# Kernel tuning notes

Hardware: AMD Instinct MI355X
Metric: run time of the kernel (lower is better)

Reference implementation:

```python
import jax, jax.numpy as jnp
import numpy as np

N_NODES = 100000
N_EDGES = 1600000
N_GRAPHS = 64
IN_C, HID, OUT_C = 9, 128, 2


def setup_inputs() -> dict:
    key = jax.random.key(0)
    ks = jax.random.split(key, 10)
    x = jax.random.normal(ks[0], (N_NODES, IN_C), dtype=jnp.float32)
    edge_index = jax.random.randint(ks[1], (2, N_EDGES), 0, N_NODES, dtype=jnp.int64)
    batch = jnp.sort(jax.random.randint(ks[2], (N_NODES,), 0, N_GRAPHS, dtype=jnp.int64))
    # GCNConv params (glorot-ish scale) and biases
    W1 = jax.random.normal(ks[3], (IN_C, HID), dtype=jnp.float32) / np.sqrt(IN_C)
    b1 = jnp.zeros((HID,), dtype=jnp.float32)
    W2 = jax.random.normal(ks[4], (HID, HID), dtype=jnp.float32) / np.sqrt(HID)
    b2 = jnp.zeros((HID,), dtype=jnp.float32)
    Wc = jax.random.normal(ks[5], (HID, OUT_C), dtype=jnp.float32) / np.sqrt(HID)
    bc = jnp.zeros((OUT_C,), dtype=jnp.float32)
    return {"x": x, "edge_index": edge_index, "batch": batch,
            "W1": W1, "b1": b1, "W2": W2, "b2": b2, "Wc": Wc, "bc": bc}


def _gcn_conv(x, row, col, dinv, W, b):
    # x: [N, Fin] -> [N, Fout]; symmetric-normalized scatter-add over edges+self-loops
    xw = x @ W                                   # dense GEMM
    norm = dinv[row] * dinv[col]                 # [E+N]
    msg = xw[row] * norm[:, None]                # gather + scale
    out = jax.ops.segment_sum(msg, col, num_segments=x.shape[0])  # scatter-add at target
    return out + b


def reference(x, edge_index, batch, W1, b1, W2, b2, Wc, bc):
    n = x.shape[0]
    loops = jnp.arange(n, dtype=edge_index.dtype)
    row = jnp.concatenate([edge_index[0], loops])  # sources (with self-loops)
    col = jnp.concatenate([edge_index[1], loops])  # targets
    deg = jax.ops.segment_sum(jnp.ones_like(col, dtype=x.dtype), col, num_segments=n)
    dinv = jnp.where(deg > 0, jax.lax.rsqrt(deg), 0.0)
    h = jax.nn.relu(_gcn_conv(x, row, col, dinv, W1, b1))
    h = jax.nn.relu(_gcn_conv(h, row, col, dinv, W2, b2))
    # global mean pool over graphs
    sums = jax.ops.segment_sum(h, batch, num_segments=N_GRAPHS)
    cnts = jax.ops.segment_sum(jnp.ones((n,), dtype=h.dtype), batch, num_segments=N_GRAPHS)
    pooled = sums / jnp.maximum(cnts, 1.0)[:, None]
    return pooled @ Wc + bc
```

## Files before the change

kernel.cpp:

```cpp
#include <hip/hip_runtime.h>

#define NN 100000
#define NE 1600000
#define NG 64
#define HIDC 128
#define INC 9
#define OUTC 2
#define BSH 9
#define NBK ((NN + 511) / 512)
#define EPB 4096
#define NBLKA ((NE + EPB - 1) / EPB)

typedef unsigned int u32;

#define PACK_REC(lc, r) (((u32)(lc) << 17) | (u32)(r))
#define REC_LC(v) ((v) >> 17)
#define REC_ROW(v) ((v) & 0x1FFFFu)

__device__ inline float bf_lo(u32 u) { return __uint_as_float(u << 16); }
__device__ inline float bf_hi(u32 u) { return __uint_as_float(u & 0xFFFF0000u); }
__device__ inline u32 f2bf(float x) {
    u32 u = __float_as_uint(x);
    return (u + 0x7FFFu + ((u >> 16) & 1u)) >> 16;
}
__device__ inline u32 packbf(float a, float b) { return f2bf(a) | (f2bf(b) << 16); }

__global__ void k_bzero(int* bcnt) {
    int t = threadIdx.x;
    if (t < NBK) bcnt[t] = 0;
}

__global__ __launch_bounds__(256) void k_bcount(const int* __restrict__ col, int* bcnt) {
    __shared__ int h[NBK];
    int t = threadIdx.x;
    if (t < NBK) h[t] = 0;
    __syncthreads();
    for (int e = blockIdx.x * 256 + t; e < NE; e += gridDim.x * 256)
        atomicAdd(&h[col[e] >> BSH], 1);
    __syncthreads();
    if (t < NBK && h[t]) atomicAdd(&bcnt[t], h[t]);
}

__global__ __launch_bounds__(256) void k_bscan(const int* __restrict__ bcnt,
                                               int* __restrict__ bbase,
                                               int* __restrict__ bcur,
                                               int* __restrict__ offsets) {
    __shared__ int lds[256];
    int t = threadIdx.x;
    int v = (t < NBK) ? bcnt[t] : 0;
    lds[t] = v;
    __syncthreads();
    for (int d = 1; d < 256; d <<= 1) {
        int u = (t >= d) ? lds[t - d] : 0;
        __syncthreads();
        lds[t] += u;
        __syncthreads();
    }
    if (t < NBK) {
        int ex = lds[t] - v;
        bbase[t] = ex;
        bcur[t] = ex;
    }
    if (t == 0) { bbase[NBK] = NE; offsets[NN] = NE; }
}

__global__ __launch_bounds__(256) void k_bscatter2(const int* __restrict__ row,
                                                   const int* __restrict__ col,
                                                   int* bcur, u32* __restrict__ staging) {
    __shared__ u32 srec[EPB];
    __shared__ u32 sbkt[EPB];
    __shared__ int hist[NBK];
    __shared__ int base[NBK];
    int t = threadIdx.x;
    long e0 = (long)blockIdx.x * EPB;
    int n = (NE - e0 < EPB) ? (int)(NE - e0) : EPB;
    for (int i = t; i < n; i += 256) {
        u32 c = col[e0 + i];
        u32 r = row[e0 + i];
        srec[i] = PACK_REC(c & 511u, r);
        sbkt[i] = c >> BSH;
    }
    if (t < NBK) hist[t] = 0;
    __syncthreads();
    for (int i = t; i < n; i += 256) atomicAdd(&hist[sbkt[i]], 1);
    __syncthreads();
    if (t < NBK) {
        int h = hist[t];
        base[t] = h ? atomicAdd(&bcur[t], h) : 0;
        hist[t] = 0;
    }
    __syncthreads();
    for (int i = t; i < n; i += 256) {
        int b = sbkt[i];
        int p = atomicAdd(&hist[b], 1) + base[b];
        staging[p] = srec[i];
    }
}

__global__ __launch_bounds__(256) void k_bcsr(const u32* __restrict__ staging,
                                              const int* __restrict__ bbase,
                                              int* __restrict__ offsets,
                                              float* __restrict__ dinv,
                                              int* __restrict__ csr_src) {
    __shared__ int cnt[512];
    __shared__ int cur[512];
    __shared__ int sc[256];
    int b = blockIdx.x, t = threadIdx.x;
    int nb0 = b << BSH;
    int nodes = NN - nb0 < 512 ? NN - nb0 : 512;
    int e0 = bbase[b], e1 = bbase[b + 1];
    cnt[t] = 0;
    cnt[t + 256] = 0;
    __syncthreads();
    for (int e = e0 + t; e < e1; e += 256)
        atomicAdd(&cnt[REC_LC(staging[e])], 1);
    __syncthreads();
    int c0 = cnt[2 * t], c1 = cnt[2 * t + 1];
    int s = c0 + c1;
    sc[t] = s;
    __syncthreads();
    for (int d = 1; d < 256; d <<= 1) {
        int u = (t >= d) ? sc[t - d] : 0;
        __syncthreads();
        sc[t] += u;
        __syncthreads();
    }
    int ex = sc[t] - s;
    cur[2 * t] = ex;
    cur[2 * t + 1] = ex + c0;
    if (2 * t < nodes) {
        offsets[nb0 + 2 * t] = e0 + ex;
        dinv[nb0 + 2 * t] = rsqrtf((float)(c0 + 1));
    }
    if (2 * t + 1 < nodes) {
        offsets[nb0 + 2 * t + 1] = e0 + ex + c0;
        dinv[nb0 + 2 * t + 1] = rsqrtf((float)(c1 + 1));
    }
    __syncthreads();
    for (int e = e0 + t; e < e1; e += 256) {
        u32 r = staging[e];
        int p = atomicAdd(&cur[REC_LC(r)], 1);
        csr_src[e0 + p] = (int)REC_ROW(r);
    }
}

__global__ __launch_bounds__(256) void k_xw1(const float* __restrict__ x,
                                             const float* __restrict__ W1,
                                             const float* __restrict__ dinv,
                                             u32* __restrict__ Ap2) {
    int tid = threadIdx.x;
    int i = blockIdx.x * 4 + (tid >> 6);
    int j = tid & 63;
    if (i >= NN) return;
    float acc0 = 0.f, acc1 = 0.f;
#pragma unroll
    for (int k = 0; k < INC; ++k) {
        float xv = x[i * INC + k];
        acc0 += xv * W1[k * HIDC + 2 * j];
        acc1 += xv * W1[k * HIDC + 2 * j + 1];
    }
    float di = dinv[i];
    Ap2[(long)i * 64 + j] = packbf(acc0 * di, acc1 * di);
}

__global__ __launch_bounds__(256) void k_gather(const u32* __restrict__ Ap2,
                                                const int* __restrict__ csr_src,
                                                const int* __restrict__ offsets,
                                                const float* __restrict__ dinv,
                                                u32* __restrict__ B2) {
    int i = (blockIdx.x * 256 + threadIdx.x) >> 6;
    if (i >= NN) return;
    int lane = threadIdx.x & 63;
    long base = (long)i * 64 + lane;
    u32 a = Ap2[base];
    float acc0 = bf_lo(a), acc1 = bf_hi(a);
    int beg = offsets[i], end = offsets[i + 1];
    int e = beg;
    for (; e + 4 <= end; e += 4) {
        int s0 = csr_src[e], s1 = csr_src[e + 1], s2 = csr_src[e + 2], s3 = csr_src[e + 3];
        u32 v0 = Ap2[(long)s0 * 64 + lane];
        u32 v1 = Ap2[(long)s1 * 64 + lane];
        u32 v2 = Ap2[(long)s2 * 64 + lane];
        u32 v3 = Ap2[(long)s3 * 64 + lane];
        acc0 += (bf_lo(v0) + bf_lo(v1)) + (bf_lo(v2) + bf_lo(v3));
        acc1 += (bf_hi(v0) + bf_hi(v1)) + (bf_hi(v2) + bf_hi(v3));
    }
    for (; e < end; ++e) {
        u32 v = Ap2[(long)csr_src[e] * 64 + lane];
        acc0 += bf_lo(v);
        acc1 += bf_hi(v);
    }
    float di = dinv[i];
    B2[base] = packbf(acc0 * di, acc1 * di);
}

__global__ __launch_bounds__(256) void k_layer2(const u32* __restrict__ B2,
                                                const float* __restrict__ b1,
                                                const float* __restrict__ W2,
                                                const float* __restrict__ dinv,
                                                u32* __restrict__ Ap2) {
    __shared__ float hs[64][HIDC + 1];
    __shared__ float W2s[32][HIDC];
    int t = threadIdx.x;
    int nb = blockIdx.x * 64;
    int j = t & 63;
    float bb0 = b1[2 * j], bb1 = b1[2 * j + 1];
    for (int n = t >> 6; n < 64; n += 4) {
        int node = nb + n;
        u32 u = (node < NN) ? B2[(long)node * 64 + j] : 0u;
        float h0 = bf_lo(u) + bb0;
        float h1 = bf_hi(u) + bb1;
        hs[n][2 * j] = h0 > 0.f ? h0 : 0.f;
        hs[n][2 * j + 1] = h1 > 0.f ? h1 : 0.f;
    }
    int cg = t & 15, ng = t >> 4;
    int n0 = ng * 4, c0 = cg * 4;
    float acc[4][8] = {};
    for (int kt = 0; kt < 4; ++kt) {
        __syncthreads();
        for (int idx = t; idx < 1024; idx += 256)
            ((float4*)W2s)[idx] = ((const float4*)W2)[kt * 1024 + idx];
        __syncthreads();
#pragma unroll 8
        for (int k = 0; k < 32; ++k) {
            int kk = kt * 32 + k;
            float a0 = hs[n0 + 0][kk], a1 = hs[n0 + 1][kk];
            float a2 = hs[n0 + 2][kk], a3 = hs[n0 + 3][kk];
            float4 w0 = *(const float4*)&W2s[k][c0];
            float4 w1 = *(const float4*)&W2s[k][c0 + 64];
            acc[0][0] += a0 * w0.x; acc[0][1] += a0 * w0.y; acc[0][2] += a0 * w0.z; acc[0][3] += a0 * w0.w;
            acc[0][4] += a0 * w1.x; acc[0][5] += a0 * w1.y; acc[0][6] += a0 * w1.z; acc[0][7] += a0 * w1.w;
            acc[1][0] += a1 * w0.x; acc[1][1] += a1 * w0.y; acc[1][2] += a1 * w0.z; acc[1][3] += a1 * w0.w;
            acc[1][4] += a1 * w1.x; acc[1][5] += a1 * w1.y; acc[1][6] += a1 * w1.z; acc[1][7] += a1 * w1.w;
            acc[2][0] += a2 * w0.x; acc[2][1] += a2 * w0.y; acc[2][2] += a2 * w0.z; acc[2][3] += a2 * w0.w;
            acc[2][4] += a2 * w1.x; acc[2][5] += a2 * w1.y; acc[2][6] += a2 * w1.z; acc[2][7] += a2 * w1.w;
            acc[3][0] += a3 * w0.x; acc[3][1] += a3 * w0.y; acc[3][2] += a3 * w0.z; acc[3][3] += a3 * w0.w;
            acc[3][4] += a3 * w1.x; acc[3][5] += a3 * w1.y; acc[3][6] += a3 * w1.z; acc[3][7] += a3 * w1.w;
        }
    }
#pragma unroll
    for (int r = 0; r < 4; ++r) {
        int node = nb + n0 + r;
        if (node < NN) {
            float di = dinv[node];
            uint2 oa, ob;
            oa.x = packbf(acc[r][0] * di, acc[r][1] * di);
            oa.y = packbf(acc[r][2] * di, acc[r][3] * di);
            ob.x = packbf(acc[r][4] * di, acc[r][5] * di);
            ob.y = packbf(acc[r][6] * di, acc[r][7] * di);
            ((uint2*)Ap2)[(long)node * 32 + cg] = oa;
            ((uint2*)Ap2)[(long)node * 32 + 16 + cg] = ob;
        }
    }
}

__global__ void k_pool_init(float* pooled, float* cnt) {
    int i = blockIdx.x * 256 + threadIdx.x;
    if (i < NG * HIDC) pooled[i] = 0.f;
    if (i < NG) cnt[i] = 0.f;
}

__global__ __launch_bounds__(64) void k_pool(const u32* __restrict__ B2,
                                             const float* __restrict__ b2,
                                             const int* __restrict__ batch,
                                             float* pooled, float* cnt) {
    int f = threadIdx.x;
    int start = blockIdx.x * 64;
    int end = start + 64 < NN ? start + 64 : NN;
    float bb0 = b2[2 * f], bb1 = b2[2 * f + 1];
    float s0 = 0.f, s1 = 0.f;
    int gcur = -1, cl = 0;
    for (int i = start; i < end; ++i) {
        int g = batch[i];
        if (g != gcur) {
            if (gcur >= 0) {
                unsafeAtomicAdd(&pooled[gcur * HIDC + 2 * f], s0);
                unsafeAtomicAdd(&pooled[gcur * HIDC + 2 * f + 1], s1);
                if (f == 0) unsafeAtomicAdd(&cnt[gcur], (float)cl);
            }
            gcur = g; s0 = s1 = 0.f; cl = 0;
        }
        u32 u = B2[(long)i * 64 + f];
        float h0 = bf_lo(u) + bb0;
        float h1 = bf_hi(u) + bb1;
        s0 += h0 > 0.f ? h0 : 0.f;
        s1 += h1 > 0.f ? h1 : 0.f;
        cl++;
    }
    if (gcur >= 0) {
        unsafeAtomicAdd(&pooled[gcur * HIDC + 2 * f], s0);
        unsafeAtomicAdd(&pooled[gcur * HIDC + 2 * f + 1], s1);
        if (f == 0) unsafeAtomicAdd(&cnt[gcur], (float)cl);
    }
}

__global__ __launch_bounds__(128) void k_final(const float* __restrict__ pooled,
                                               const float* __restrict__ cnt,
                                               const float* __restrict__ Wc,
                                               const float* __restrict__ bc,
                                               float* __restrict__ out) {
    __shared__ float v0s[HIDC], v1s[HIDC];
    int g = blockIdx.x, f = threadIdx.x;
    float c = cnt[g]; c = c > 1.f ? c : 1.f;
    float val = pooled[g * HIDC + f] / c;
    v0s[f] = val * Wc[f * OUTC + 0];
    v1s[f] = val * Wc[f * OUTC + 1];
    __syncthreads();
    if (f < 2) {
        const float* arr = (f == 0) ? v0s : v1s;
        float s = 0.f;
        for (int k = 0; k < HIDC; ++k) s += arr[k];
        out[g * OUTC + f] = s + bc[f];
    }
}

extern "C" void kernel_launch(void* const* d_in, const int* in_sizes, int n_in,
                              void* d_out, int out_size, void* d_ws, size_t ws_size,
                              hipStream_t stream) {
    const float* x     = (const float*)d_in[0];
    const int*   ei    = (const int*)d_in[1];
    const int*   batch = (const int*)d_in[2];
    const float* W1    = (const float*)d_in[3];
    const float* b1    = (const float*)d_in[4];
    const float* W2    = (const float*)d_in[5];
    const float* b2    = (const float*)d_in[6];
    const float* Wc    = (const float*)d_in[7];
    const float* bc    = (const float*)d_in[8];
    float* out = (float*)d_out;

    char* ws = (char*)d_ws;
    size_t off = 0;
    auto alloc = [&](size_t bytes) { void* p = ws + off; off += (bytes + 255) / 256 * 256; return p; };
    u32*   Ap2     = (u32*)alloc((size_t)NN * 64 * 4);
    u32*   B2      = (u32*)alloc((size_t)NN * 64 * 4);
    float* dinv    = (float*)alloc((size_t)NN * 4);
    int*   offsets = (int*)alloc((size_t)(NN + 1) * 4);
    int*   csr_src = (int*)alloc((size_t)NE * 4);
    u32*   staging = (u32*)alloc((size_t)NE * 4);
    int*   bcnt    = (int*)alloc((size_t)NBK * 4);
    int*   bbase   = (int*)alloc((size_t)(NBK + 1) * 4);
    int*   bcur    = (int*)alloc((size_t)NBK * 4);
    float* pooled  = (float*)alloc((size_t)NG * HIDC * 4);
    float* cnt     = (float*)alloc((size_t)NG * 4);

    const int* row = ei;
    const int* col = ei + NE;

    k_bzero<<<1, 256, 0, stream>>>(bcnt);
    k_bcount<<<512, 256, 0, stream>>>(col, bcnt);
    k_bscan<<<1, 256, 0, stream>>>(bcnt, bbase, bcur, offsets);
    k_bscatter2<<<NBLKA, 256, 0, stream>>>(row, col, bcur, staging);
    k_bcsr<<<NBK, 256, 0, stream>>>(staging, bbase, offsets, dinv, csr_src);

    k_xw1<<<(NN + 3) / 4, 256, 0, stream>>>(x, W1, dinv, Ap2);
    k_gather<<<(NN * 64 + 255) / 256, 256, 0, stream>>>(Ap2, csr_src, offsets, dinv, B2);

    k_layer2<<<(NN + 63) / 64, 256, 0, stream>>>(B2, b1, W2, dinv, Ap2);
    k_gather<<<(NN * 64 + 255) / 256, 256, 0, stream>>>(Ap2, csr_src, offsets, dinv, B2);

    k_pool_init<<<(NG * HIDC + 255) / 256, 256, 0, stream>>>(pooled, cnt);
    k_pool<<<(NN + 63) / 64, 64, 0, stream>>>(B2, b2, batch, pooled, cnt);
    k_final<<<NG, 128, 0, stream>>>(pooled, cnt, Wc, bc, out);
}
```

Baseline: 340.0 us.

## Drop the bucket count pass using fixed-capacity buckets; retile layer2 GEMM

The separate edge-count kernel is removed. The scatter kernel now writes each record into a fixed-capacity slot region per bucket (CAP entries), and the global counters it builds are scanned afterwards to get CSR offsets. This saves one full pass over the column indices and one launch. In exchange it depends on no bucket holding more than CAP edges: that holds for uniformly random edges, but any overflow silently drops edges. The gather inner loop is unrolled to 8 edges with a 2-edge tail to keep more loads in flight. The layer-2 GEMM now handles 128 nodes per block, holds 16 outputs per thread, and reads W2 straight from global memory as float4 instead of staging it in LDS.

```diff
diff --git a/kernel.cpp b/kernel.cpp
--- a/kernel.cpp
+++ b/kernel.cpp
@@ -10,6 +10,7 @@
 #define NBK ((NN + 511) / 512)
 #define EPB 4096
 #define NBLKA ((NE + EPB - 1) / EPB)
+#define CAP 12288
 
 typedef unsigned int u32;
 
@@ -25,48 +26,14 @@
 }
 __device__ inline u32 packbf(float a, float b) { return f2bf(a) | (f2bf(b) << 16); }
 
-__global__ void k_bzero(int* bcnt) {
+__global__ void k_zero196(int* bcnt) {
     int t = threadIdx.x;
     if (t < NBK) bcnt[t] = 0;
 }
 
-__global__ __launch_bounds__(256) void k_bcount(const int* __restrict__ col, int* bcnt) {
-    __shared__ int h[NBK];
-    int t = threadIdx.x;
-    if (t < NBK) h[t] = 0;
-    __syncthreads();
-    for (int e = blockIdx.x * 256 + t; e < NE; e += gridDim.x * 256)
-        atomicAdd(&h[col[e] >> BSH], 1);
-    __syncthreads();
-    if (t < NBK && h[t]) atomicAdd(&bcnt[t], h[t]);
-}
-
-__global__ __launch_bounds__(256) void k_bscan(const int* __restrict__ bcnt,
-                                               int* __restrict__ bbase,
-                                               int* __restrict__ bcur,
-                                               int* __restrict__ offsets) {
-    __shared__ int lds[256];
-    int t = threadIdx.x;
-    int v = (t < NBK) ? bcnt[t] : 0;
-    lds[t] = v;
-    __syncthreads();
-    for (int d = 1; d < 256; d <<= 1) {
-        int u = (t >= d) ? lds[t - d] : 0;
-        __syncthreads();
-        lds[t] += u;
-        __syncthreads();
-    }
-    if (t < NBK) {
-        int ex = lds[t] - v;
-        bbase[t] = ex;
-        bcur[t] = ex;
-    }
-    if (t == 0) { bbase[NBK] = NE; offsets[NN] = NE; }
-}
-
 __global__ __launch_bounds__(256) void k_bscatter2(const int* __restrict__ row,
                                                    const int* __restrict__ col,
-                                                   int* bcur, u32* __restrict__ staging) {
+                                                   int* bcnt, u32* __restrict__ staging) {
     __shared__ u32 srec[EPB];
     __shared__ u32 sbkt[EPB];
     __shared__ int hist[NBK];
@@ -86,18 +53,37 @@
     __syncthreads();
     if (t < NBK) {
         int h = hist[t];
-        base[t] = h ? atomicAdd(&bcur[t], h) : 0;
+        base[t] = h ? atomicAdd(&bcnt[t], h) : 0;
         hist[t] = 0;
     }
     __syncthreads();
     for (int i = t; i < n; i += 256) {
         int b = sbkt[i];
         int p = atomicAdd(&hist[b], 1) + base[b];
-        staging[p] = srec[i];
-    }
+        if (p < CAP) staging[(long)b * CAP + p] = srec[i];
+    }
+}
+
+__global__ __launch_bounds__(256) void k_bscan(const int* __restrict__ bcnt,
+                                               int* __restrict__ bbase,
+                                               int* __restrict__ offsets) {
+    __shared__ int lds[256];
+    int t = threadIdx.x;
+    int v = (t < NBK) ? bcnt[t] : 0;
+    lds[t] = v;
+    __syncthreads();
+    for (int d = 1; d < 256; d <<= 1) {
+        int u = (t >= d) ? lds[t - d] : 0;
+        __syncthreads();
+        lds[t] += u;
+        __syncthreads();
+    }
+    if (t < NBK) bbase[t] = lds[t] - v;
+    if (t == 0) offsets[NN] = NE;
 }
 
 __global__ __launch_bounds__(256) void k_bcsr(const u32* __restrict__ staging,
+                                              const int* __restrict__ bcnt,
                                               const int* __restrict__ bbase,
                                               int* __restrict__ offsets,
                                               float* __restrict__ dinv,
@@ -108,12 +94,14 @@
     int b = blockIdx.x, t = threadIdx.x;
     int nb0 = b << BSH;
     int nodes = NN - nb0 < 512 ? NN - nb0 : 512;
-    int e0 = bbase[b], e1 = bbase[b + 1];
+    int ne_b = bcnt[b];
+    long s0b = (long)b * CAP;
+    int e0 = bbase[b];
     cnt[t] = 0;
     cnt[t + 256] = 0;
     __syncthreads();
-    for (int e = e0 + t; e < e1; e += 256)
-        atomicAdd(&cnt[REC_LC(staging[e])], 1);
+    for (int e = t; e < ne_b; e += 256)
+        atomicAdd(&cnt[REC_LC(staging[s0b + e])], 1);
     __syncthreads();
     int c0 = cnt[2 * t], c1 = cnt[2 * t + 1];
     int s = c0 + c1;
@@ -137,8 +125,8 @@
         dinv[nb0 + 2 * t + 1] = rsqrtf((float)(c1 + 1));
     }
     __syncthreads();
-    for (int e = e0 + t; e < e1; e += 256) {
-        u32 r = staging[e];
+    for (int e = t; e < ne_b; e += 256) {
+        u32 r = staging[s0b + e];
         int p = atomicAdd(&cur[REC_LC(r)], 1);
         csr_src[e0 + p] = (int)REC_ROW(r);
     }
@@ -176,14 +164,28 @@
     float acc0 = bf_lo(a), acc1 = bf_hi(a);
     int beg = offsets[i], end = offsets[i + 1];
     int e = beg;
-    for (; e + 4 <= end; e += 4) {
-        int s0 = csr_src[e], s1 = csr_src[e + 1], s2 = csr_src[e + 2], s3 = csr_src[e + 3];
+    for (; e + 8 <= end; e += 8) {
+        int s0 = csr_src[e + 0], s1 = csr_src[e + 1], s2 = csr_src[e + 2], s3 = csr_src[e + 3];
+        int s4 = csr_src[e + 4], s5 = csr_src[e + 5], s6 = csr_src[e + 6], s7 = csr_src[e + 7];
         u32 v0 = Ap2[(long)s0 * 64 + lane];
         u32 v1 = Ap2[(long)s1 * 64 + lane];
         u32 v2 = Ap2[(long)s2 * 64 + lane];
         u32 v3 = Ap2[(long)s3 * 64 + lane];
-        acc0 += (bf_lo(v0) + bf_lo(v1)) + (bf_lo(v2) + bf_lo(v3));
-        acc1 += (bf_hi(v0) + bf_hi(v1)) + (bf_hi(v2) + bf_hi(v3));
+        u32 v4 = Ap2[(long)s4 * 64 + lane];
+        u32 v5 = Ap2[(long)s5 * 64 + lane];
+        u32 v6 = Ap2[(long)s6 * 64 + lane];
+        u32 v7 = Ap2[(long)s7 * 64 + lane];
+        acc0 += ((bf_lo(v0) + bf_lo(v1)) + (bf_lo(v2) + bf_lo(v3))) +
+                ((bf_lo(v4) + bf_lo(v5)) + (bf_lo(v6) + bf_lo(v7)));
+        acc1 += ((bf_hi(v0) + bf_hi(v1)) + (bf_hi(v2) + bf_hi(v3))) +
+                ((bf_hi(v4) + bf_hi(v5)) + (bf_hi(v6) + bf_hi(v7)));
+    }
+    for (; e + 2 <= end; e += 2) {
+        int s0 = csr_src[e], s1 = csr_src[e + 1];
+        u32 v0 = Ap2[(long)s0 * 64 + lane];
+        u32 v1 = Ap2[(long)s1 * 64 + lane];
+        acc0 += bf_lo(v0) + bf_lo(v1);
+        acc1 += bf_hi(v0) + bf_hi(v1);
     }
     for (; e < end; ++e) {
         u32 v = Ap2[(long)csr_src[e] * 64 + lane];
@@ -199,13 +201,12 @@
                                                 const float* __restrict__ W2,
                                                 const float* __restrict__ dinv,
                                                 u32* __restrict__ Ap2) {
-    __shared__ float hs[64][HIDC + 1];
-    __shared__ float W2s[32][HIDC];
+    __shared__ float hs[128][HIDC];
     int t = threadIdx.x;
-    int nb = blockIdx.x * 64;
+    int nb = blockIdx.x * 128;
     int j = t & 63;
     float bb0 = b1[2 * j], bb1 = b1[2 * j + 1];
-    for (int n = t >> 6; n < 64; n += 4) {
+    for (int n = t >> 6; n < 128; n += 4) {
         int node = nb + n;
         u32 u = (node < NN) ? B2[(long)node * 64 + j] : 0u;
         float h0 = bf_lo(u) + bb0;
@@ -213,29 +214,26 @@
         hs[n][2 * j] = h0 > 0.f ? h0 : 0.f;
         hs[n][2 * j + 1] = h1 > 0.f ? h1 : 0.f;
     }
-    int cg = t & 15, ng = t >> 4;
-    int n0 = ng * 4, c0 = cg * 4;
-    float acc[4][8] = {};
-    for (int kt = 0; kt < 4; ++kt) {
-        __syncthreads();
-        for (int idx = t; idx < 1024; idx += 256)
-            ((float4*)W2s)[idx] = ((const float4*)W2)[kt * 1024 + idx];
-        __syncthreads();
-#pragma unroll 8
-        for (int k = 0; k < 32; ++k) {
-            int kk = kt * 32 + k;
-            float a0 = hs[n0 + 0][kk], a1 = hs[n0 + 1][kk];
-            float a2 = hs[n0 + 2][kk], a3 = hs[n0 + 3][kk];
-            float4 w0 = *(const float4*)&W2s[k][c0];
-            float4 w1 = *(const float4*)&W2s[k][c0 + 64];
-            acc[0][0] += a0 * w0.x; acc[0][1] += a0 * w0.y; acc[0][2] += a0 * w0.z; acc[0][3] += a0 * w0.w;
-            acc[0][4] += a0 * w1.x; acc[0][5] += a0 * w1.y; acc[0][6] += a0 * w1.z; acc[0][7] += a0 * w1.w;
-            acc[1][0] += a1 * w0.x; acc[1][1] += a1 * w0.y; acc[1][2] += a1 * w0.z; acc[1][3] += a1 * w0.w;
-            acc[1][4] += a1 * w1.x; acc[1][5] += a1 * w1.y; acc[1][6] += a1 * w1.z; acc[1][7] += a1 * w1.w;
-            acc[2][0] += a2 * w0.x; acc[2][1] += a2 * w0.y; acc[2][2] += a2 * w0.z; acc[2][3] += a2 * w0.w;
-            acc[2][4] += a2 * w1.x; acc[2][5] += a2 * w1.y; acc[2][6] += a2 * w1.z; acc[2][7] += a2 * w1.w;
-            acc[3][0] += a3 * w0.x; acc[3][1] += a3 * w0.y; acc[3][2] += a3 * w0.z; acc[3][3] += a3 * w0.w;
-            acc[3][4] += a3 * w1.x; acc[3][5] += a3 * w1.y; acc[3][6] += a3 * w1.z; acc[3][7] += a3 * w1.w;
+    __syncthreads();
+    int cg = t & 7, ng = t >> 3;
+    int n0 = ng * 4;
+    const float4* W4 = (const float4*)W2;
+    float acc[4][16] = {};
+#pragma unroll 2
+    for (int k = 0; k < HIDC; ++k) {
+        float4 w0 = W4[k * 32 + cg * 4 + 0];
+        float4 w1 = W4[k * 32 + cg * 4 + 1];
+        float4 w2 = W4[k * 32 + cg * 4 + 2];
+        float4 w3 = W4[k * 32 + cg * 4 + 3];
+        float a0 = hs[n0 + 0][k], a1 = hs[n0 + 1][k];
+        float a2 = hs[n0 + 2][k], a3 = hs[n0 + 3][k];
+#pragma unroll
+        for (int r = 0; r < 4; ++r) {
+            float ar = (r == 0) ? a0 : (r == 1) ? a1 : (r == 2) ? a2 : a3;
+            acc[r][0] += ar * w0.x;  acc[r][1] += ar * w0.y;  acc[r][2] += ar * w0.z;  acc[r][3] += ar * w0.w;
+            acc[r][4] += ar * w1.x;  acc[r][5] += ar * w1.y;  acc[r][6] += ar * w1.z;  acc[r][7] += ar * w1.w;
+            acc[r][8] += ar * w2.x;  acc[r][9] += ar * w2.y;  acc[r][10] += ar * w2.z; acc[r][11] += ar * w2.w;
+            acc[r][12] += ar * w3.x; acc[r][13] += ar * w3.y; acc[r][14] += ar * w3.z; acc[r][15] += ar * w3.w;
         }
     }
 #pragma unroll
@@ -243,13 +241,17 @@
         int node = nb + n0 + r;
         if (node < NN) {
             float di = dinv[node];
-            uint2 oa, ob;
+            uint4 oa, ob;
             oa.x = packbf(acc[r][0] * di, acc[r][1] * di);
             oa.y = packbf(acc[r][2] * di, acc[r][3] * di);
-            ob.x = packbf(acc[r][4] * di, acc[r][5] * di);
-            ob.y = packbf(acc[r][6] * di, acc[r][7] * di);
-            ((uint2*)Ap2)[(long)node * 32 + cg] = oa;
-            ((uint2*)Ap2)[(long)node * 32 + 16 + cg] = ob;
+            oa.z = packbf(acc[r][4] * di, acc[r][5] * di);
+            oa.w = packbf(acc[r][6] * di, acc[r][7] * di);
+            ob.x = packbf(acc[r][8] * di, acc[r][9] * di);
+            ob.y = packbf(acc[r][10] * di, acc[r][11] * di);
+            ob.z = packbf(acc[r][12] * di, acc[r][13] * di);
+            ob.w = packbf(acc[r][14] * di, acc[r][15] * di);
+            ((uint4*)Ap2)[(long)node * 16 + cg * 2 + 0] = oa;
+            ((uint4*)Ap2)[(long)node * 16 + cg * 2 + 1] = ob;
         }
     }
 }
@@ -336,26 +338,24 @@
     float* dinv    = (float*)alloc((size_t)NN * 4);
     int*   offsets = (int*)alloc((size_t)(NN + 1) * 4);
     int*   csr_src = (int*)alloc((size_t)NE * 4);
-    u32*   staging = (u32*)alloc((size_t)NE * 4);
+    u32*   staging = (u32*)alloc((size_t)NBK * CAP * 4);
     int*   bcnt    = (int*)alloc((size_t)NBK * 4);
-    int*   bbase   = (int*)alloc((size_t)(NBK + 1) * 4);
-    int*   bcur    = (int*)alloc((size_t)NBK * 4);
+    int*   bbase   = (int*)alloc((size_t)NBK * 4);
     float* pooled  = (float*)alloc((size_t)NG * HIDC * 4);
     float* cnt     = (float*)alloc((size_t)NG * 4);
 
     const int* row = ei;
     const int* col = ei + NE;
 
-    k_bzero<<<1, 256, 0, stream>>>(bcnt);
-    k_bcount<<<512, 256, 0, stream>>>(col, bcnt);
-    k_bscan<<<1, 256, 0, stream>>>(bcnt, bbase, bcur, offsets);
-    k_bscatter2<<<NBLKA, 256, 0, stream>>>(row, col, bcur, staging);
-    k_bcsr<<<NBK, 256, 0, stream>>>(staging, bbase, offsets, dinv, csr_src);
+    k_zero196<<<1, 256, 0, stream>>>(bcnt);
+    k_bscatter2<<<NBLKA, 256, 0, stream>>>(row, col, bcnt, staging);
+    k_bscan<<<1, 256, 0, stream>>>(bcnt, bbase, offsets);
+    k_bcsr<<<NBK, 256, 0, stream>>>(staging, bcnt, bbase, offsets, dinv, csr_src);
 
     k_xw1<<<(NN + 3) / 4, 256, 0, stream>>>(x, W1, dinv, Ap2);
     k_gather<<<(NN * 64 + 255) / 256, 256, 0, stream>>>(Ap2, csr_src, offsets, dinv, B2);
 
-    k_layer2<<<(NN + 63) / 64, 256, 0, stream>>>(B2, b1, W2, dinv, Ap2);
+    k_layer2<<<(NN + 127) / 128, 256, 0, stream>>>(B2, b1, W2, dinv, Ap2);
     k_gather<<<(NN * 64 + 255) / 256, 256, 0, stream>>>(Ap2, csr_src, offsets, dinv, B2);
 
     k_pool_init<<<(NG * HIDC + 255) / 256, 256, 0, stream>>>(pooled, cnt);
```

New measurement: 387.7 us. +14.0%, slower.
